# Kernel tuning notes

Measured on AMD Instinct MI355X. Metric: run time of the kernel, lower is better.

The kernel has to match this reference:

```python
import jax, jax.numpy as jnp
import numpy as np

N_NODES = 50000
N_EDGES = 800000
IN_DIM = 256
HID = 256
OUT = 2


def setup_inputs() -> dict:
    key = jax.random.key(0)
    ks = jax.random.split(key, 12)
    x = jax.random.normal(ks[0], (N_NODES, IN_DIM), dtype=jnp.float32)
    edge_index = jax.random.randint(ks[1], (2, N_EDGES), 0, N_NODES, dtype=jnp.int64)
    s = lambda fan_in: 1.0 / np.sqrt(fan_in)
    return {
        "x": x,
        "edge_index": edge_index,
        # SAGEConv 1: lin_l (neighbors, with bias), lin_r (root, no bias)
        "W1l": jax.random.normal(ks[2], (IN_DIM, HID), dtype=jnp.float32) * s(IN_DIM),
        "b1l": jnp.zeros((HID,), dtype=jnp.float32),
        "W1r": jax.random.normal(ks[3], (IN_DIM, HID), dtype=jnp.float32) * s(IN_DIM),
        # SAGEConv 2
        "W2l": jax.random.normal(ks[4], (HID, HID), dtype=jnp.float32) * s(HID),
        "b2l": jnp.zeros((HID,), dtype=jnp.float32),
        "W2r": jax.random.normal(ks[5], (HID, HID), dtype=jnp.float32) * s(HID),
        # edge MLP: Linear(2H -> H), ReLU, Linear(H -> OUT)
        "Wm1": jax.random.normal(ks[6], (2 * HID, HID), dtype=jnp.float32) * s(2 * HID),
        "bm1": jnp.zeros((HID,), dtype=jnp.float32),
        "Wm2": jax.random.normal(ks[7], (HID, OUT), dtype=jnp.float32) * s(HID),
        "bm2": jnp.zeros((OUT,), dtype=jnp.float32),
    }


def _sage_conv(x, src, dst, Wl, bl, Wr):
    # mean-aggregate source features at destination nodes (PyG SAGEConv, aggr='mean')
    n = x.shape[0]
    msg_sum = jax.ops.segment_sum(x[src], dst, num_segments=n)      # [N, D]
    deg = jax.ops.segment_sum(jnp.ones((src.shape[0],), x.dtype), dst, num_segments=n)
    agg = msg_sum / jnp.maximum(deg, 1.0)[:, None]
    return agg @ Wl + bl + x @ Wr


def reference(x, edge_index, W1l, b1l, W1r, W2l, b2l, W2r, Wm1, bm1, Wm2, bm2):
    src, dst = edge_index[0], edge_index[1]
    h = jax.nn.relu(_sage_conv(x, src, dst, W1l, b1l, W1r))
    h = jax.nn.relu(_sage_conv(h, src, dst, W2l, b2l, W2r))
    edge_reps = jnp.concatenate([h[src], h[dst]], axis=1)           # [E, 2H]
    hidden = jax.nn.relu(edge_reps @ Wm1 + bm1)
    logits = hidden @ Wm2 + bm2                                     # [E, OUT]
    return logits
```

## Files before the change

### kernel.cpp

```cpp
#include <hip/hip_runtime.h>

#define IN_DIM 256
#define HID 256
#define SCAN_CHUNK 512
#define PADW 264

typedef unsigned short ushort_t;
typedef __attribute__((ext_vector_type(8))) short short8;
typedef __attribute__((ext_vector_type(4))) float floatx4;

__device__ __forceinline__ float b2f(ushort_t h) {
    union { unsigned int u; float f; } c; c.u = ((unsigned int)h) << 16; return c.f;
}
__device__ __forceinline__ ushort_t f2b(float f) {
    union { float f; unsigned int u; } c; c.f = f;
    unsigned int u = c.u;
    unsigned int r = (u + 0x7fffu + ((u >> 16) & 1u)) >> 16;
    return (ushort_t)r;
}

__global__ void k_count_deg(const int* __restrict__ dst, int* __restrict__ deg, int E) {
    int e = blockIdx.x * blockDim.x + threadIdx.x;
    if (e < E) atomicAdd(&deg[dst[e]], 1);
}

__global__ __launch_bounds__(64) void k_chunk_sum(const int* __restrict__ deg,
                                                  int* __restrict__ partials, int N) {
    int lane = threadIdx.x;
    int base = blockIdx.x * SCAN_CHUNK + lane * 8;
    int s = 0;
#pragma unroll
    for (int i = 0; i < 8; ++i) s += (base + i < N) ? deg[base + i] : 0;
#pragma unroll
    for (int off = 32; off > 0; off >>= 1) s += __shfl_down(s, off, 64);
    if (lane == 0) partials[blockIdx.x] = s;
}

__global__ void k_scan_partials(int* __restrict__ partials, int nb) {
    if (threadIdx.x == 0 && blockIdx.x == 0) {
        int run = 0;
        for (int i = 0; i < nb; ++i) { int v = partials[i]; partials[i] = run; run += v; }
    }
}

__global__ __launch_bounds__(64) void k_scan_chunks(const int* __restrict__ deg,
                                                    const int* __restrict__ partials,
                                                    int* __restrict__ row_start,
                                                    int* __restrict__ cursor, int N) {
    int lane = threadIdx.x;
    int base = blockIdx.x * SCAN_CHUNK + lane * 8;
    int v[8]; int lsum = 0;
#pragma unroll
    for (int i = 0; i < 8; ++i) { v[i] = (base + i < N) ? deg[base + i] : 0; lsum += v[i]; }
    int pre = lsum;
#pragma unroll
    for (int off = 1; off < 64; off <<= 1) {
        int t = __shfl_up(pre, off, 64);
        if (lane >= off) pre += t;
    }
    pre -= lsum;
    int run = partials[blockIdx.x] + pre;
#pragma unroll
    for (int i = 0; i < 8; ++i) {
        if (base + i < N) { row_start[base + i] = run; cursor[base + i] = run; }
        run += v[i];
    }
}

__global__ void k_bucket(const int* __restrict__ src, const int* __restrict__ dst,
                         int* __restrict__ cursor, int2* __restrict__ csr, int E) {
    int e = blockIdx.x * blockDim.x + threadIdx.x;
    if (e < E) {
        int pos = atomicAdd(&cursor[dst[e]], 1);
        csr[pos] = make_int2(src[e], e);
    }
}

__global__ __launch_bounds__(256) void k_cast(const float* __restrict__ x,
                                              ushort_t* __restrict__ xb, int n4) {
    int i = blockIdx.x * blockDim.x + threadIdx.x;
    if (i >= n4) return;
    float4 v = ((const float4*)x)[i];
    ushort4 o;
    o.x = f2b(v.x); o.y = f2b(v.y); o.z = f2b(v.z); o.w = f2b(v.w);
    ((ushort4*)xb)[i] = o;
}

__global__ __launch_bounds__(64) void k_wprep(const float* __restrict__ Wsrc,
                                              ushort_t* __restrict__ WF,
                                              int nbTot, int nb0) {
    int lane = threadIdx.x;
    int kb = blockIdx.x >> 4, nbL = blockIdx.x & 15;
    int k = kb * 32 + (lane >> 4) * 8;
    int n = nbL * 16 + (lane & 15);
    size_t dstb = (size_t)(kb * nbTot + nb0 + nbL) * 512 + lane * 8;
#pragma unroll
    for (int j = 0; j < 8; ++j) {
        WF[dstb + j] = f2b(Wsrc[(size_t)(k + j) * 256 + n]);
    }
}

__global__ __launch_bounds__(256) void k_gather(const ushort_t* __restrict__ X,
                                                const int2* __restrict__ csr,
                                                const int* __restrict__ row_start,
                                                const int* __restrict__ deg,
                                                ushort_t* __restrict__ agg, int N) {
    int lane = threadIdx.x & 63;
    int node = blockIdx.x * 4 + (threadIdx.x >> 6);
    if (node >= N) return;
    int quad = lane >> 4, l16 = lane & 15;
    int start = row_start[node];
    int cnt = deg[node];
    const int2* sp = csr + start;
    float acc[16] = {};
    for (int b = 0; b < cnt; b += 64) {
        int nb = min(64, cnt - b);
        int sidx = (lane < nb) ? sp[b + lane].x : 0;
        for (int j8 = 0; j8 < nb; j8 += 8) {
            int jA = j8 + quad, jB = j8 + 4 + quad;
            bool vA = jA < nb, vB = jB < nb;
            int sA = __shfl(sidx, vA ? jA : 0, 64);
            int sB = __shfl(sidx, vB ? jB : 0, 64);
            const ushort_t* rowA = X + (size_t)sA * HID + l16 * 16;
            const ushort_t* rowB = X + (size_t)sB * HID + l16 * 16;
            short8 a0 = *(const short8*)(rowA);
            short8 a1 = *(const short8*)(rowA + 8);
            short8 b0 = *(const short8*)(rowB);
            short8 b1 = *(const short8*)(rowB + 8);
            if (vA) {
#pragma unroll
                for (int i = 0; i < 8; ++i) {
                    acc[i]     += b2f((ushort_t)a0[i]);
                    acc[8 + i] += b2f((ushort_t)a1[i]);
                }
            }
            if (vB) {
#pragma unroll
                for (int i = 0; i < 8; ++i) {
                    acc[i]     += b2f((ushort_t)b0[i]);
                    acc[8 + i] += b2f((ushort_t)b1[i]);
                }
            }
        }
    }
#pragma unroll
    for (int i = 0; i < 16; ++i) {
        acc[i] += __shfl_down(acc[i], 32, 64);
        acc[i] += __shfl_down(acc[i], 16, 64);
    }
    if (quad == 0) {
        float sc = 1.0f / (float)max(cnt, 1);
        short8 o0, o1;
#pragma unroll
        for (int i = 0; i < 8; ++i) {
            o0[i] = (short)f2b(acc[i] * sc);
            o1[i] = (short)f2b(acc[8 + i] * sc);
        }
        ushort_t* op = agg + (size_t)node * HID + l16 * 16;
        *(short8*)(op) = o0;
        *(short8*)(op + 8) = o1;
    }
}

__global__ __launch_bounds__(256) void k_mfma(const ushort_t* __restrict__ A1,
                                              const ushort_t* __restrict__ WF1,
                                              const ushort_t* __restrict__ A2,
                                              const ushort_t* __restrict__ WF2,
                                              const float* __restrict__ bias, int relu,
                                              int M, int nbTot,
                                              ushort_t* __restrict__ C,
                                              ushort_t* __restrict__ C2) {
    __shared__ ushort_t As[64 * PADW];
    const int tid = threadIdx.x;
    const int lane = tid & 63;
    const int w = tid >> 6;
    const int wm = w >> 1, wn = w & 1;
    const int quad = lane >> 4, l16 = lane & 15;
    const int m0 = blockIdx.y * 64;
    const int n0 = blockIdx.x * 64;
    const int nbBase = (n0 >> 4) + wn * 2;

    floatx4 acc[2][2] = {};

    for (int op = 0; op < 2; ++op) {
        const ushort_t* A = op ? A2 : A1;
        const ushort_t* WF = op ? WF2 : WF1;
        if (A == nullptr) continue;
        if (op) __syncthreads();
#pragma unroll
        for (int i = 0; i < 8; ++i) {
            int c = i * 256 + tid;
            int row = c >> 5, col = c & 31;
            int arow = m0 + row; if (arow >= M) arow = M - 1;
            *(uint4*)&As[row * PADW + col * 8] =
                *(const uint4*)(A + (size_t)arow * 256 + col * 8);
        }
        __syncthreads();

        const ushort_t* a0p = &As[(wm * 32 + l16) * PADW + quad * 8];
        const ushort_t* a1p = a0p + 16 * PADW;
        const ushort_t* wp = WF + (size_t)nbBase * 512 + lane * 8;
#pragma unroll
        for (int kb = 0; kb < 8; ++kb) {
            short8 a0 = *(const short8*)(a0p + kb * 32);
            short8 a1 = *(const short8*)(a1p + kb * 32);
            const ushort_t* wkb = wp + (size_t)kb * nbTot * 512;
            short8 b0 = *(const short8*)(wkb);
            short8 b1 = *(const short8*)(wkb + 512);
            acc[0][0] = __builtin_amdgcn_mfma_f32_16x16x32_bf16(a0, b0, acc[0][0], 0, 0, 0);
            acc[0][1] = __builtin_amdgcn_mfma_f32_16x16x32_bf16(a0, b1, acc[0][1], 0, 0, 0);
            acc[1][0] = __builtin_amdgcn_mfma_f32_16x16x32_bf16(a1, b0, acc[1][0], 0, 0, 0);
            acc[1][1] = __builtin_amdgcn_mfma_f32_16x16x32_bf16(a1, b1, acc[1][1], 0, 0, 0);
        }
    }

#pragma unroll
    for (int mi = 0; mi < 2; ++mi) {
#pragma unroll
        for (int nj = 0; nj < 2; ++nj) {
            int col = n0 + wn * 32 + nj * 16 + l16;
            float b = bias ? bias[col] : 0.f;
            int rbase = m0 + wm * 32 + mi * 16 + quad * 4;
            ushort_t* dstp = C;
            int c = col;
            if (C2 && col >= 256) { dstp = C2; c = col - 256; }
#pragma unroll
            for (int reg = 0; reg < 4; ++reg) {
                int r = rbase + reg;
                if (r >= M) continue;
                float v = acc[mi][nj][reg] + b;
                if (relu) v = fmaxf(v, 0.f);
                dstp[(size_t)r * 256 + c] = f2b(v);
            }
        }
    }
}

__global__ __launch_bounds__(256) void k_edge(const ushort_t* __restrict__ P,
                                              const ushort_t* __restrict__ Q,
                                              const int2* __restrict__ csr,
                                              const int* __restrict__ row_start,
                                              const int* __restrict__ deg,
                                              const float* __restrict__ bm1,
                                              const float* __restrict__ Wm2,
                                              const float* __restrict__ bm2,
                                              float* __restrict__ out, int N, int stride) {
    int lane = threadIdx.x & 63;
    int wid = blockIdx.x * 4 + (threadIdx.x >> 6);
    int half = lane >> 5, l32 = lane & 31;

    float w0[8], w1[8], bb[8];
    const float* bp = bm1 + l32 * 8;
    const float2* wp = (const float2*)Wm2 + l32 * 8;
#pragma unroll
    for (int i = 0; i < 8; ++i) {
        float2 wv = wp[i];
        w0[i] = wv.x; w1[i] = wv.y;
        bb[i] = bp[i];
    }
    float bo0 = bm2[0], bo1 = bm2[1];

    for (int node = wid; node < N; node += stride) {
        int start = row_start[node];
        int cnt = deg[node];
        if (cnt == 0) continue;

        short8 qv = *(const short8*)(Q + (size_t)node * HID + l32 * 8);
        float qb[8];
#pragma unroll
        for (int i = 0; i < 8; ++i) qb[i] = b2f((ushort_t)qv[i]) + bb[i];

        const int2* sp = csr + start;
        for (int b = 0; b < cnt; b += 64) {
            int nb = min(64, cnt - b);
            int2 se = (lane < nb) ? sp[b + lane] : make_int2(0, 0);
            for (int j0 = 0; j0 < nb; j0 += 8) {
                int jA = j0 + half, jB = j0 + 2 + half, jC = j0 + 4 + half, jD = j0 + 6 + half;
                bool vA = jA < nb, vB = jB < nb, vC = jC < nb, vD = jD < nb;
                int iA = vA ? jA : 0, iB = vB ? jB : 0, iC = vC ? jC : 0, iD = vD ? jD : 0;
                int sA = __shfl(se.x, iA, 64);
                int sB = __shfl(se.x, iB, 64);
                int sC = __shfl(se.x, iC, 64);
                int sD = __shfl(se.x, iD, 64);
                short8 pA = *(const short8*)(P + (size_t)sA * HID + l32 * 8);
                short8 pB = *(const short8*)(P + (size_t)sB * HID + l32 * 8);
                short8 pC = *(const short8*)(P + (size_t)sC * HID + l32 * 8);
                short8 pD = *(const short8*)(P + (size_t)sD * HID + l32 * 8);
                float aA0 = 0.f, aA1 = 0.f, aB0 = 0.f, aB1 = 0.f;
                float aC0 = 0.f, aC1 = 0.f, aD0 = 0.f, aD1 = 0.f;
#pragma unroll
                for (int i = 0; i < 8; ++i) {
                    float hA = fmaxf(b2f((ushort_t)pA[i]) + qb[i], 0.f);
                    float hB = fmaxf(b2f((ushort_t)pB[i]) + qb[i], 0.f);
                    float hC = fmaxf(b2f((ushort_t)pC[i]) + qb[i], 0.f);
                    float hD = fmaxf(b2f((ushort_t)pD[i]) + qb[i], 0.f);
                    aA0 += hA * w0[i]; aA1 += hA * w1[i];
                    aB0 += hB * w0[i]; aB1 += hB * w1[i];
                    aC0 += hC * w0[i]; aC1 += hC * w1[i];
                    aD0 += hD * w0[i]; aD1 += hD * w1[i];
                }
#pragma unroll
                for (int off = 16; off > 0; off >>= 1) {
                    aA0 += __shfl_down(aA0, off, 32);
                    aA1 += __shfl_down(aA1, off, 32);
                    aB0 += __shfl_down(aB0, off, 32);
                    aB1 += __shfl_down(aB1, off, 32);
                    aC0 += __shfl_down(aC0, off, 32);
                    aC1 += __shfl_down(aC1, off, 32);
                    aD0 += __shfl_down(aD0, off, 32);
                    aD1 += __shfl_down(aD1, off, 32);
                }
                int eA = __shfl(se.y, iA, 64);
                int eB = __shfl(se.y, iB, 64);
                int eC = __shfl(se.y, iC, 64);
                int eD = __shfl(se.y, iD, 64);
                if (l32 == 0) {
                    if (vA) { float2 o; o.x = aA0 + bo0; o.y = aA1 + bo1; ((float2*)out)[eA] = o; }
                    if (vB) { float2 o; o.x = aB0 + bo0; o.y = aB1 + bo1; ((float2*)out)[eB] = o; }
                    if (vC) { float2 o; o.x = aC0 + bo0; o.y = aC1 + bo1; ((float2*)out)[eC] = o; }
                    if (vD) { float2 o; o.x = aD0 + bo0; o.y = aD1 + bo1; ((float2*)out)[eD] = o; }
                }
            }
        }
    }
}

extern "C" void kernel_launch(void* const* d_in, const int* in_sizes, int n_in,
                              void* d_out, int out_size, void* d_ws, size_t ws_size,
                              hipStream_t stream) {
    const float* x   = (const float*)d_in[0];
    const int*   ei  = (const int*)d_in[1];
    const float* W1l = (const float*)d_in[2];
    const float* b1l = (const float*)d_in[3];
    const float* W1r = (const float*)d_in[4];
    const float* W2l = (const float*)d_in[5];
    const float* b2l = (const float*)d_in[6];
    const float* W2r = (const float*)d_in[7];
    const float* Wm1 = (const float*)d_in[8];
    const float* bm1 = (const float*)d_in[9];
    const float* Wm2 = (const float*)d_in[10];
    const float* bm2 = (const float*)d_in[11];

    const int N = in_sizes[0] / IN_DIM;
    const int E = in_sizes[1] / 2;
    const int* src = ei;
    const int* dst = ei + E;
    const int NB = (N + SCAN_CHUNK - 1) / SCAN_CHUNK;

    char* ws = (char*)d_ws;
    size_t off = 0;
    auto alloc = [&](size_t bytes) { void* p = ws + off; off = (off + bytes + 255) & ~(size_t)255; return p; };
    int* deg       = (int*)alloc((size_t)N * 4);
    int* row_start = (int*)alloc((size_t)N * 4);
    int* cursor    = (int*)alloc((size_t)N * 4);
    int* partials  = (int*)alloc((size_t)(NB + 1) * 4);
    int2* csr      = (int2*)alloc((size_t)E * 8);
    size_t matB = (size_t)N * HID * sizeof(ushort_t);
    ushort_t* xb   = (ushort_t*)alloc(matB);
    ushort_t* aggB = (ushort_t*)alloc(matB);
    ushort_t* h1b  = (ushort_t*)alloc(matB);
    ushort_t* h2b  = (ushort_t*)alloc(matB);
    ushort_t* Pb   = (ushort_t*)alloc(matB);
    ushort_t* Qb   = (ushort_t*)alloc(matB);
    size_t wfB  = (size_t)8 * 16 * 512 * sizeof(ushort_t);
    ushort_t* WF1l = (ushort_t*)alloc(wfB);
    ushort_t* WF1r = (ushort_t*)alloc(wfB);
    ushort_t* WF2l = (ushort_t*)alloc(wfB);
    ushort_t* WF2r = (ushort_t*)alloc(wfB);
    ushort_t* WFm  = (ushort_t*)alloc(wfB * 2);
    float* out = (float*)d_out;

    int nwg = (N + 3) / 4;
    int mrows = (N + 63) / 64;

    hipMemsetAsync(deg, 0, (size_t)N * 4, stream);
    k_count_deg<<<(E + 255) / 256, 256, 0, stream>>>(dst, deg, E);
    k_chunk_sum<<<NB, 64, 0, stream>>>(deg, partials, N);
    k_scan_partials<<<1, 64, 0, stream>>>(partials, NB);
    k_scan_chunks<<<NB, 64, 0, stream>>>(deg, partials, row_start, cursor, N);
    k_bucket<<<(E + 255) / 256, 256, 0, stream>>>(src, dst, cursor, csr, E);

    k_cast<<<(N * HID / 4 + 255) / 256, 256, 0, stream>>>(x, xb, N * HID / 4);
    k_wprep<<<128, 64, 0, stream>>>(W1l, WF1l, 16, 0);
    k_wprep<<<128, 64, 0, stream>>>(W1r, WF1r, 16, 0);
    k_wprep<<<128, 64, 0, stream>>>(W2l, WF2l, 16, 0);
    k_wprep<<<128, 64, 0, stream>>>(W2r, WF2r, 16, 0);
    k_wprep<<<128, 64, 0, stream>>>(Wm1, WFm, 32, 0);
    k_wprep<<<128, 64, 0, stream>>>(Wm1 + (size_t)256 * 256, WFm, 32, 16);

    k_gather<<<nwg, 256, 0, stream>>>(xb, csr, row_start, deg, aggB, N);
    k_mfma<<<dim3(4, mrows), 256, 0, stream>>>(aggB, WF1l, xb, WF1r, b1l, 1, N, 16, h1b, nullptr);

    k_gather<<<nwg, 256, 0, stream>>>(h1b, csr, row_start, deg, aggB, N);
    k_mfma<<<dim3(4, mrows), 256, 0, stream>>>(aggB, WF2l, h1b, WF2r, b2l, 1, N, 16, h2b, nullptr);

    k_mfma<<<dim3(8, mrows), 256, 0, stream>>>(h2b, WFm, nullptr, nullptr, nullptr, 0, N, 32, Pb, Qb);

    const int EB = 2048;
    k_edge<<<EB, 256, 0, stream>>>(Pb, Qb, csr, row_start, deg, bm1, Wm2, bm2, out, N, EB * 4);
}
```

Baseline: 564.5 us.

## Widen MFMA tile so each block computes 256 output columns

Each block of the bf16 MFMA GEMM now covers a 64x256 output tile instead of 64x64, with each wave owning 16 rows and all 16 column blocks. The A tile is loaded into shared memory once per 256 columns rather than once per 64 columns, which cuts the redundant A reads and staging. The trade-off is a 4x smaller grid, 16 accumulator vectors per thread (more register pressure, lower occupancy) and more weight loads from global memory per wave.

New measurement: 630.2 us. +11.6%, slower.

```diff
diff --git a/kernel.cpp b/kernel.cpp
--- a/kernel.cpp
+++ b/kernel.cpp
@@ -174,13 +174,11 @@
     const int tid = threadIdx.x;
     const int lane = tid & 63;
     const int w = tid >> 6;
-    const int wm = w >> 1, wn = w & 1;
     const int quad = lane >> 4, l16 = lane & 15;
     const int m0 = blockIdx.y * 64;
-    const int n0 = blockIdx.x * 64;
-    const int nbBase = (n0 >> 4) + wn * 2;
-
-    floatx4 acc[2][2] = {};
+    const int nb0 = blockIdx.x * 16;
+
+    floatx4 acc[16] = {};
 
     for (int op = 0; op < 2; ++op) {
         const ushort_t* A = op ? A2 : A1;
@@ -197,41 +195,34 @@
         }
         __syncthreads();
 
-        const ushort_t* a0p = &As[(wm * 32 + l16) * PADW + quad * 8];
-        const ushort_t* a1p = a0p + 16 * PADW;
-        const ushort_t* wp = WF + (size_t)nbBase * 512 + lane * 8;
+        const ushort_t* ap = &As[(w * 16 + l16) * PADW + quad * 8];
 #pragma unroll
         for (int kb = 0; kb < 8; ++kb) {
-            short8 a0 = *(const short8*)(a0p + kb * 32);
-            short8 a1 = *(const short8*)(a1p + kb * 32);
-            const ushort_t* wkb = wp + (size_t)kb * nbTot * 512;
-            short8 b0 = *(const short8*)(wkb);
-            short8 b1 = *(const short8*)(wkb + 512);
-            acc[0][0] = __builtin_amdgcn_mfma_f32_16x16x32_bf16(a0, b0, acc[0][0], 0, 0, 0);
-            acc[0][1] = __builtin_amdgcn_mfma_f32_16x16x32_bf16(a0, b1, acc[0][1], 0, 0, 0);
-            acc[1][0] = __builtin_amdgcn_mfma_f32_16x16x32_bf16(a1, b0, acc[1][0], 0, 0, 0);
-            acc[1][1] = __builtin_amdgcn_mfma_f32_16x16x32_bf16(a1, b1, acc[1][1], 0, 0, 0);
-        }
-    }
-
-#pragma unroll
-    for (int mi = 0; mi < 2; ++mi) {
-#pragma unroll
-        for (int nj = 0; nj < 2; ++nj) {
-            int col = n0 + wn * 32 + nj * 16 + l16;
-            float b = bias ? bias[col] : 0.f;
-            int rbase = m0 + wm * 32 + mi * 16 + quad * 4;
-            ushort_t* dstp = C;
-            int c = col;
-            if (C2 && col >= 256) { dstp = C2; c = col - 256; }
-#pragma unroll
-            for (int reg = 0; reg < 4; ++reg) {
-                int r = rbase + reg;
-                if (r >= M) continue;
-                float v = acc[mi][nj][reg] + b;
-                if (relu) v = fmaxf(v, 0.f);
-                dstp[(size_t)r * 256 + c] = f2b(v);
+            short8 a = *(const short8*)(ap + kb * 32);
+            const ushort_t* wkb = WF + (size_t)(kb * nbTot + nb0) * 512 + lane * 8;
+#pragma unroll
+            for (int nb = 0; nb < 16; ++nb) {
+                short8 b = *(const short8*)(wkb + nb * 512);
+                acc[nb] = __builtin_amdgcn_mfma_f32_16x16x32_bf16(a, b, acc[nb], 0, 0, 0);
             }
+        }
+    }
+
+    int rbase = m0 + w * 16 + quad * 4;
+#pragma unroll
+    for (int nb = 0; nb < 16; ++nb) {
+        int col = (nb0 + nb) * 16 + l16;
+        float bv = bias ? bias[col] : 0.f;
+        ushort_t* dstp = C;
+        int c = col;
+        if (C2 && col >= 256) { dstp = C2; c = col - 256; }
+#pragma unroll
+        for (int reg = 0; reg < 4; ++reg) {
+            int r = rbase + reg;
+            if (r >= M) continue;
+            float v = acc[nb][reg] + bv;
+            if (relu) v = fmaxf(v, 0.f);
+            dstp[(size_t)r * 256 + c] = f2b(v);
         }
     }
 }
@@ -389,12 +380,12 @@
     k_wprep<<<128, 64, 0, stream>>>(Wm1 + (size_t)256 * 256, WFm, 32, 16);
 
     k_gather<<<nwg, 256, 0, stream>>>(xb, csr, row_start, deg, aggB, N);
-    k_mfma<<<dim3(4, mrows), 256, 0, stream>>>(aggB, WF1l, xb, WF1r, b1l, 1, N, 16, h1b, nullptr);
+    k_mfma<<<dim3(1, mrows), 256, 0, stream>>>(aggB, WF1l, xb, WF1r, b1l, 1, N, 16, h1b, nullptr);
 
     k_gather<<<nwg, 256, 0, stream>>>(h1b, csr, row_start, deg, aggB, N);
-    k_mfma<<<dim3(4, mrows), 256, 0, stream>>>(aggB, WF2l, h1b, WF2r, b2l, 1, N, 16, h2b, nullptr);
-
-    k_mfma<<<dim3(8, mrows), 256, 0, stream>>>(h2b, WFm, nullptr, nullptr, nullptr, 0, N, 32, Pb, Qb);
+    k_mfma<<<dim3(1, mrows), 256, 0, stream>>>(aggB, WF2l, h1b, WF2r, b2l, 1, N, 16, h2b, nullptr);
+
+    k_mfma<<<dim3(2, mrows), 256, 0, stream>>>(h2b, WFm, nullptr, nullptr, nullptr, 0, N, 32, Pb, Qb);
 
     const int EB = 2048;
     k_edge<<<EB, 256, 0, stream>>>(Pb, Qb, csr, row_start, deg, bm1, Wm2, bm2, out, N, EB * 4);
```

## Split gather and edge kernels into two 128-column feature passes

Applied to the files above, without the earlier changes.

Both the neighbor-mean gather kernel and the fused edge-MLP kernel now walk the graph twice, each pass covering half of the 256 feature columns. The aim is to halve the randomly gathered working set per pass so more of it stays in cache. In exchange, edge indices are re-read and re-shuffled twice, per-lane loads in the edge kernel shrink to 8 bytes, and the output is written in the first pass and read back and updated in the second.

Measured after the change: 655.3 us. 1.16x slower.

```diff
diff --git a/kernel.cpp b/kernel.cpp
--- a/kernel.cpp
+++ b/kernel.cpp
@@ -112,53 +112,41 @@
     int start = row_start[node];
     int cnt = deg[node];
     const int2* sp = csr + start;
-    float acc[16] = {};
-    for (int b = 0; b < cnt; b += 64) {
-        int nb = min(64, cnt - b);
-        int sidx = (lane < nb) ? sp[b + lane].x : 0;
-        for (int j8 = 0; j8 < nb; j8 += 8) {
-            int jA = j8 + quad, jB = j8 + 4 + quad;
-            bool vA = jA < nb, vB = jB < nb;
-            int sA = __shfl(sidx, vA ? jA : 0, 64);
-            int sB = __shfl(sidx, vB ? jB : 0, 64);
-            const ushort_t* rowA = X + (size_t)sA * HID + l16 * 16;
-            const ushort_t* rowB = X + (size_t)sB * HID + l16 * 16;
-            short8 a0 = *(const short8*)(rowA);
-            short8 a1 = *(const short8*)(rowA + 8);
-            short8 b0 = *(const short8*)(rowB);
-            short8 b1 = *(const short8*)(rowB + 8);
-            if (vA) {
-#pragma unroll
-                for (int i = 0; i < 8; ++i) {
-                    acc[i]     += b2f((ushort_t)a0[i]);
-                    acc[8 + i] += b2f((ushort_t)a1[i]);
+    float sc = 1.0f / (float)max(cnt, 1);
+    for (int ph = 0; ph < 2; ++ph) {
+        int coff = ph * 128 + l16 * 8;
+        float acc[8] = {};
+        for (int b = 0; b < cnt; b += 64) {
+            int nb = min(64, cnt - b);
+            int sidx = (lane < nb) ? sp[b + lane].x : 0;
+            for (int j8 = 0; j8 < nb; j8 += 8) {
+                int jA = j8 + quad, jB = j8 + 4 + quad;
+                bool vA = jA < nb, vB = jB < nb;
+                int sA = __shfl(sidx, vA ? jA : 0, 64);
+                int sB = __shfl(sidx, vB ? jB : 0, 64);
+                short8 a0 = *(const short8*)(X + (size_t)sA * HID + coff);
+                short8 b0 = *(const short8*)(X + (size_t)sB * HID + coff);
+                if (vA) {
+#pragma unroll
+                    for (int i = 0; i < 8; ++i) acc[i] += b2f((ushort_t)a0[i]);
+                }
+                if (vB) {
+#pragma unroll
+                    for (int i = 0; i < 8; ++i) acc[i] += b2f((ushort_t)b0[i]);
                 }
             }
-            if (vB) {
-#pragma unroll
-                for (int i = 0; i < 8; ++i) {
-                    acc[i]     += b2f((ushort_t)b0[i]);
-                    acc[8 + i] += b2f((ushort_t)b1[i]);
-                }
-            }
-        }
-    }
-#pragma unroll
-    for (int i = 0; i < 16; ++i) {
-        acc[i] += __shfl_down(acc[i], 32, 64);
-        acc[i] += __shfl_down(acc[i], 16, 64);
-    }
-    if (quad == 0) {
-        float sc = 1.0f / (float)max(cnt, 1);
-        short8 o0, o1;
+        }
 #pragma unroll
         for (int i = 0; i < 8; ++i) {
-            o0[i] = (short)f2b(acc[i] * sc);
-            o1[i] = (short)f2b(acc[8 + i] * sc);
-        }
-        ushort_t* op = agg + (size_t)node * HID + l16 * 16;
-        *(short8*)(op) = o0;
-        *(short8*)(op + 8) = o1;
+            acc[i] += __shfl_down(acc[i], 32, 64);
+            acc[i] += __shfl_down(acc[i], 16, 64);
+        }
+        if (quad == 0) {
+            short8 o;
+#pragma unroll
+            for (int i = 0; i < 8; ++i) o[i] = (short)f2b(acc[i] * sc);
+            *(short8*)(agg + (size_t)node * HID + coff) = o;
+        }
     }
 }
 
@@ -249,76 +237,115 @@
     int wid = blockIdx.x * 4 + (threadIdx.x >> 6);
     int half = lane >> 5, l32 = lane & 31;
 
-    float w0[8], w1[8], bb[8];
-    const float* bp = bm1 + l32 * 8;
-    const float2* wp = (const float2*)Wm2 + l32 * 8;
-#pragma unroll
-    for (int i = 0; i < 8; ++i) {
-        float2 wv = wp[i];
-        w0[i] = wv.x; w1[i] = wv.y;
-        bb[i] = bp[i];
+    float w0[2][4], w1[2][4], bb[2][4];
+#pragma unroll
+    for (int ph = 0; ph < 2; ++ph) {
+        const float* bp = bm1 + ph * 128 + l32 * 4;
+        const float2* wp = (const float2*)Wm2 + ph * 128 + l32 * 4;
+#pragma unroll
+        for (int i = 0; i < 4; ++i) {
+            float2 wv = wp[i];
+            w0[ph][i] = wv.x; w1[ph][i] = wv.y;
+            bb[ph][i] = bp[i];
+        }
     }
     float bo0 = bm2[0], bo1 = bm2[1];
 
-    for (int node = wid; node < N; node += stride) {
-        int start = row_start[node];
-        int cnt = deg[node];
-        if (cnt == 0) continue;
-
-        short8 qv = *(const short8*)(Q + (size_t)node * HID + l32 * 8);
-        float qb[8];
-#pragma unroll
-        for (int i = 0; i < 8; ++i) qb[i] = b2f((ushort_t)qv[i]) + bb[i];
-
-        const int2* sp = csr + start;
-        for (int b = 0; b < cnt; b += 64) {
-            int nb = min(64, cnt - b);
-            int2 se = (lane < nb) ? sp[b + lane] : make_int2(0, 0);
-            for (int j0 = 0; j0 < nb; j0 += 8) {
-                int jA = j0 + half, jB = j0 + 2 + half, jC = j0 + 4 + half, jD = j0 + 6 + half;
-                bool vA = jA < nb, vB = jB < nb, vC = jC < nb, vD = jD < nb;
-                int iA = vA ? jA : 0, iB = vB ? jB : 0, iC = vC ? jC : 0, iD = vD ? jD : 0;
-                int sA = __shfl(se.x, iA, 64);
-                int sB = __shfl(se.x, iB, 64);
-                int sC = __shfl(se.x, iC, 64);
-                int sD = __shfl(se.x, iD, 64);
-                short8 pA = *(const short8*)(P + (size_t)sA * HID + l32 * 8);
-                short8 pB = *(const short8*)(P + (size_t)sB * HID + l32 * 8);
-                short8 pC = *(const short8*)(P + (size_t)sC * HID + l32 * 8);
-                short8 pD = *(const short8*)(P + (size_t)sD * HID + l32 * 8);
-                float aA0 = 0.f, aA1 = 0.f, aB0 = 0.f, aB1 = 0.f;
-                float aC0 = 0.f, aC1 = 0.f, aD0 = 0.f, aD1 = 0.f;
-#pragma unroll
-                for (int i = 0; i < 8; ++i) {
-                    float hA = fmaxf(b2f((ushort_t)pA[i]) + qb[i], 0.f);
-                    float hB = fmaxf(b2f((ushort_t)pB[i]) + qb[i], 0.f);
-                    float hC = fmaxf(b2f((ushort_t)pC[i]) + qb[i], 0.f);
-                    float hD = fmaxf(b2f((ushort_t)pD[i]) + qb[i], 0.f);
-                    aA0 += hA * w0[i]; aA1 += hA * w1[i];
-                    aB0 += hB * w0[i]; aB1 += hB * w1[i];
-                    aC0 += hC * w0[i]; aC1 += hC * w1[i];
-                    aD0 += hD * w0[i]; aD1 += hD * w1[i];
-                }
-#pragma unroll
-                for (int off = 16; off > 0; off >>= 1) {
-                    aA0 += __shfl_down(aA0, off, 32);
-                    aA1 += __shfl_down(aA1, off, 32);
-                    aB0 += __shfl_down(aB0, off, 32);
-                    aB1 += __shfl_down(aB1, off, 32);
-                    aC0 += __shfl_down(aC0, off, 32);
-                    aC1 += __shfl_down(aC1, off, 32);
-                    aD0 += __shfl_down(aD0, off, 32);
-                    aD1 += __shfl_down(aD1, off, 32);
-                }
-                int eA = __shfl(se.y, iA, 64);
-                int eB = __shfl(se.y, iB, 64);
-                int eC = __shfl(se.y, iC, 64);
-                int eD = __shfl(se.y, iD, 64);
-                if (l32 == 0) {
-                    if (vA) { float2 o; o.x = aA0 + bo0; o.y = aA1 + bo1; ((float2*)out)[eA] = o; }
-                    if (vB) { float2 o; o.x = aB0 + bo0; o.y = aB1 + bo1; ((float2*)out)[eB] = o; }
-                    if (vC) { float2 o; o.x = aC0 + bo0; o.y = aC1 + bo1; ((float2*)out)[eC] = o; }
-                    if (vD) { float2 o; o.x = aD0 + bo0; o.y = aD1 + bo1; ((float2*)out)[eD] = o; }
+    for (int ph = 0; ph < 2; ++ph) {
+        for (int node = wid; node < N; node += stride) {
+            int start = row_start[node];
+            int cnt = deg[node];
+            if (cnt == 0) continue;
+            int coff = ph * 128 + l32 * 4;
+
+            ushort4 qv = *(const ushort4*)(Q + (size_t)node * HID + coff);
+            float qb[4];
+            qb[0] = b2f(qv.x) + bb[ph][0];
+            qb[1] = b2f(qv.y) + bb[ph][1];
+            qb[2] = b2f(qv.z) + bb[ph][2];
+            qb[3] = b2f(qv.w) + bb[ph][3];
+
+            const int2* sp = csr + start;
+            for (int b = 0; b < cnt; b += 64) {
+                int nb = min(64, cnt - b);
+                int2 se = (lane < nb) ? sp[b + lane] : make_int2(0, 0);
+                for (int j0 = 0; j0 < nb; j0 += 8) {
+                    int jA = j0 + half, jB = j0 + 2 + half, jC = j0 + 4 + half, jD = j0 + 6 + half;
+                    bool vA = jA < nb, vB = jB < nb, vC = jC < nb, vD = jD < nb;
+                    int iA = vA ? jA : 0, iB = vB ? jB : 0, iC = vC ? jC : 0, iD = vD ? jD : 0;
+                    int sA = __shfl(se.x, iA, 64);
+                    int sB = __shfl(se.x, iB, 64);
+                    int sC = __shfl(se.x, iC, 64);
+                    int sD = __shfl(se.x, iD, 64);
+                    ushort4 pA = *(const ushort4*)(P + (size_t)sA * HID + coff);
+                    ushort4 pB = *(const ushort4*)(P + (size_t)sB * HID + coff);
+                    ushort4 pC = *(const ushort4*)(P + (size_t)sC * HID + coff);
+                    ushort4 pD = *(const ushort4*)(P + (size_t)sD * HID + coff);
+                    float aA0, aA1, aB0, aB1, aC0, aC1, aD0, aD1;
+                    {
+                        float h0 = fmaxf(b2f(pA.x) + qb[0], 0.f);
+                        float h1 = fmaxf(b2f(pA.y) + qb[1], 0.f);
+                        float h2 = fmaxf(b2f(pA.z) + qb[2], 0.f);
+                        float h3 = fmaxf(b2f(pA.w) + qb[3], 0.f);
+                        aA0 = h0*w0[ph][0] + h1*w0[ph][1] + h2*w0[ph][2] + h3*w0[ph][3];
+                        aA1 = h0*w1[ph][0] + h1*w1[ph][1] + h2*w1[ph][2] + h3*w1[ph][3];
+                    }
+                    {
+                        float h0 = fmaxf(b2f(pB.x) + qb[0], 0.f);
+                        float h1 = fmaxf(b2f(pB.y) + qb[1], 0.f);
+                        float h2 = fmaxf(b2f(pB.z) + qb[2], 0.f);
+                        float h3 = fmaxf(b2f(pB.w) + qb[3], 0.f);
+                        aB0 = h0*w0[ph][0] + h1*w0[ph][1] + h2*w0[ph][2] + h3*w0[ph][3];
+                        aB1 = h0*w1[ph][0] + h1*w1[ph][1] + h2*w1[ph][2] + h3*w1[ph][3];
+                    }
+                    {
+                        float h0 = fmaxf(b2f(pC.x) + qb[0], 0.f);
+                        float h1 = fmaxf(b2f(pC.y) + qb[1], 0.f);
+                        float h2 = fmaxf(b2f(pC.z) + qb[2], 0.f);
+                        float h3 = fmaxf(b2f(pC.w) + qb[3], 0.f);
+                        aC0 = h0*w0[ph][0] + h1*w0[ph][1] + h2*w0[ph][2] + h3*w0[ph][3];
+                        aC1 = h0*w1[ph][0] + h1*w1[ph][1] + h2*w1[ph][2] + h3*w1[ph][3];
+                    }
+                    {
+                        float h0 = fmaxf(b2f(pD.x) + qb[0], 0.f);
+                        float h1 = fmaxf(b2f(pD.y) + qb[1], 0.f);
+                        float h2 = fmaxf(b2f(pD.z) + qb[2], 0.f);
+                        float h3 = fmaxf(b2f(pD.w) + qb[3], 0.f);
+                        aD0 = h0*w0[ph][0] + h1*w0[ph][1] + h2*w0[ph][2] + h3*w0[ph][3];
+                        aD1 = h0*w1[ph][0] + h1*w1[ph][1] + h2*w1[ph][2] + h3*w1[ph][3];
+                    }
+#pragma unroll
+                    for (int off = 16; off > 0; off >>= 1) {
+                        aA0 += __shfl_down(aA0, off, 32);
+                        aA1 += __shfl_down(aA1, off, 32);
+                        aB0 += __shfl_down(aB0, off, 32);
+                        aB1 += __shfl_down(aB1, off, 32);
+                        aC0 += __shfl_down(aC0, off, 32);
+                        aC1 += __shfl_down(aC1, off, 32);
+                        aD0 += __shfl_down(aD0, off, 32);
+                        aD1 += __shfl_down(aD1, off, 32);
+                    }
+                    int eA = __shfl(se.y, iA, 64);
+                    int eB = __shfl(se.y, iB, 64);
+                    int eC = __shfl(se.y, iC, 64);
+                    int eD = __shfl(se.y, iD, 64);
+                    if (l32 == 0) {
+                        if (ph == 0) {
+                            if (vA) ((float2*)out)[eA] = make_float2(aA0, aA1);
+                            if (vB) ((float2*)out)[eB] = make_float2(aB0, aB1);
+                            if (vC) ((float2*)out)[eC] = make_float2(aC0, aC1);
+                            if (vD) ((float2*)out)[eD] = make_float2(aD0, aD1);
+                        } else {
+                            if (vA) { float2 o = ((float2*)out)[eA];
+                                      ((float2*)out)[eA] = make_float2(o.x + aA0 + bo0, o.y + aA1 + bo1); }
+                            if (vB) { float2 o = ((float2*)out)[eB];
+                                      ((float2*)out)[eB] = make_float2(o.x + aB0 + bo0, o.y + aB1 + bo1); }
+                            if (vC) { float2 o = ((float2*)out)[eC];
+                                      ((float2*)out)[eC] = make_float2(o.x + aC0 + bo0, o.y + aC1 + bo1); }
+                            if (vD) { float2 o = ((float2*)out)[eD];
+                                      ((float2*)out)[eD] = make_float2(o.x + aD0 + bo0, o.y + aD1 + bo1); }
+                        }
+                    }
                 }
             }
         }
```
